# Optimization experiments

Measured on AMD Instinct MI355X. Metric: run time of the kernel, lower is better.

The kernel has to match this reference:

```python
import jax, jax.numpy as jnp
import numpy as np

R, C = 30, 56
N = R * C  # 1680
K = 0.005
PRCN = 15
ALPHA = 1.0
BETA = 1.0


def setup_inputs() -> dict:
    key = jax.random.key(0)
    k1, k2 = jax.random.split(key)
    net_in = jax.random.normal(k1, (2 * N,), dtype=jnp.float32)
    # Recurrent connectivity matrix (learned weight in the original, loaded from .mat)
    J = jax.random.normal(k2, (N, N), dtype=jnp.float32) / np.float32(np.sqrt(N))
    return {"net_in": net_in, "J": J}


def reference(net_in, J):
    Iext = net_in[:N].reshape(R, C)
    r0 = net_in[N:2 * N].reshape(R, C)

    def step(r, _):
        # 4-way chunked mm + cat in the original == single matvec J @ r_flat
        temp = (J @ r.reshape(N)).reshape(R, C)
        U = ALPHA * (BETA * temp) + ALPHA * Iext
        sq = jnp.square(0.2 * U)
        recSum = jnp.sum(K * sq)
        # (0.2*U)^2 * (0.04 / recSum) / 0.04  ==  sq / recSum, kept explicit for fidelity
        r_new = sq * (0.04 / recSum) / 0.04
        return r_new, (U, recSum)

    r_last, (Us, sums) = jax.lax.scan(step, r0, None, length=PRCN - 1)
    return Us[-1], sums[-1], r_last
```

## Files before the change

kernel.cpp:

```cpp
#include <hip/hip_runtime.h>


typedef float f32x4 __attribute__((ext_vector_type(4)));

#define N      1680
#define NV4    420
#define NSTEP  14
#define GBLK   105
#define RPB    16
#define RPW    4

__device__ __forceinline__ void load7_llc(
    const f32x4* p0, const f32x4* p1, const f32x4* p2, const f32x4* p3,
    const f32x4* p4, const f32x4* p5, const f32x4* p6,
    f32x4& v0, f32x4& v1, f32x4& v2, f32x4& v3,
    f32x4& v4, f32x4& v5, f32x4& v6)
{
    asm volatile(
        "global_load_dwordx4 %0, %7, off sc0 sc1\n\t"
        "global_load_dwordx4 %1, %8, off sc0 sc1\n\t"
        "global_load_dwordx4 %2, %9, off sc0 sc1\n\t"
        "global_load_dwordx4 %3, %10, off sc0 sc1\n\t"
        "global_load_dwordx4 %4, %11, off sc0 sc1\n\t"
        "global_load_dwordx4 %5, %12, off sc0 sc1\n\t"
        "global_load_dwordx4 %6, %13, off sc0 sc1\n\t"
        "s_waitcnt vmcnt(0)"
        : "=&v"(v0), "=&v"(v1), "=&v"(v2), "=&v"(v3),
          "=&v"(v4), "=&v"(v5), "=&v"(v6)
        : "v"(p0), "v"(p1), "v"(p2), "v"(p3), "v"(p4), "v"(p5), "v"(p6)
        : "memory");
}

__device__ __forceinline__ void llc_store4(f32x4* p, f32x4 v) {
    asm volatile("global_store_dwordx4 %0, %1, off sc0 sc1"
                 :: "v"(p), "v"(v) : "memory");
}

__device__ __forceinline__ f32x4 vmin4(f32x4 a, f32x4 b) {
    f32x4 r;
    r[0] = fminf(a[0], b[0]); r[1] = fminf(a[1], b[1]);
    r[2] = fminf(a[2], b[2]); r[3] = fminf(a[3], b[3]);
    return r;
}

__global__ __launch_bounds__(256, 1) void fused_recur(
    const float* __restrict__ J,
    const float* __restrict__ net_in,
    float* __restrict__ out,
    float* __restrict__ ws)
{
    f32x4* bufs = (f32x4*)ws;

    const int tid  = threadIdx.x;
    const int lane = tid & 63;
    const int wave = tid >> 6;
    const int row0 = (int)blockIdx.x * RPB + wave * RPW;

    f32x4 Jr[RPW][7];
    #pragma unroll
    for (int m = 0; m < RPW; ++m) {
        const f32x4* Jrow = (const f32x4*)(J + (size_t)(row0 + m) * N);
        #pragma unroll
        for (int k = 0; k < 7; ++k) {
            const int idx = lane + 64 * k;
            Jr[m][k] = (idx < NV4) ? Jrow[idx] : (f32x4)0.f;
        }
    }

    float iext[RPW];
    #pragma unroll
    for (int m = 0; m < RPW; ++m) iext[m] = net_in[row0 + m];

    float Uv[RPW], Qv[RPW];

    #pragma unroll 1
    for (int t = 0; t < NSTEP; ++t) {
        #pragma unroll
        for (int m = 0; m < RPW; ++m)
            #pragma unroll
            for (int k = 0; k < 7; ++k)
                asm volatile("" : "+v"(Jr[m][k]));

        f32x4 rv[7];
        float psum = 0.0f;

        if (t == 0) {
            const f32x4* r0 = (const f32x4*)(net_in + N);
            #pragma unroll
            for (int k = 0; k < 7; ++k) {
                const int idx = lane + 64 * k;
                rv[k] = (idx < NV4) ? r0[idx] : (f32x4)0.f;
            }
        } else {
            const f32x4* base = bufs + (size_t)(t - 1) * NV4;
            const f32x4* q0 = base + (lane);
            const f32x4* q1 = base + (lane + 64);
            const f32x4* q2 = base + (lane + 128);
            const f32x4* q3 = base + (lane + 192);
            const f32x4* q4 = base + (lane + 256);
            const f32x4* q5 = base + (lane + 320);
            const f32x4* q6 = (lane < 36) ? (base + lane + 384) : base;
            for (;;) {
                load7_llc(q0, q1, q2, q3, q4, q5, q6,
                          rv[0], rv[1], rv[2], rv[3], rv[4], rv[5], rv[6]);
                f32x4 m0 = vmin4(vmin4(rv[0], rv[1]), vmin4(rv[2], rv[3]));
                f32x4 m1 = vmin4(vmin4(rv[4], rv[5]), rv[6]);
                f32x4 mm = vmin4(m0, m1);
                const float mn = fminf(fminf(mm[0], mm[1]), fminf(mm[2], mm[3]));
                if (mn >= 0.0f) break;
            }
            if (lane >= 36) rv[6] = (f32x4)0.f;
            #pragma unroll
            for (int k = 0; k < 7; ++k)
                psum += (rv[k][0] + rv[k][1]) + (rv[k][2] + rv[k][3]);
        }

        float red[5];
        #pragma unroll
        for (int m = 0; m < RPW; ++m) {
            float acc = 0.f;
            #pragma unroll
            for (int k = 0; k < 7; ++k) {
                acc += Jr[m][k][0] * rv[k][0];
                acc += Jr[m][k][1] * rv[k][1];
                acc += Jr[m][k][2] * rv[k][2];
                acc += Jr[m][k][3] * rv[k][3];
            }
            red[m] = acc;
        }
        red[4] = psum;
        #pragma unroll
        for (int off = 32; off; off >>= 1) {
            #pragma unroll
            for (int i = 0; i < 5; ++i) red[i] += __shfl_xor(red[i], off, 64);
        }
        const float s = (t == 0) ? 1.0f : 0.005f * red[4];

        #pragma unroll
        for (int m = 0; m < RPW; ++m) {
            const float U  = red[m] / s + iext[m];
            const float u2 = 0.2f * U;
            Uv[m] = U;
            Qv[m] = u2 * u2;
        }

        if (lane == 0) {
            f32x4 pub = { Qv[0], Qv[1], Qv[2], Qv[3] };
            llc_store4(bufs + (size_t)t * NV4 + (row0 >> 2), pub);
        }
    }

    float s13;
    {
        const f32x4* base = bufs + (size_t)(NSTEP - 1) * NV4;
        const f32x4* q0 = base + (lane);
        const f32x4* q1 = base + (lane + 64);
        const f32x4* q2 = base + (lane + 128);
        const f32x4* q3 = base + (lane + 192);
        const f32x4* q4 = base + (lane + 256);
        const f32x4* q5 = base + (lane + 320);
        const f32x4* q6 = (lane < 36) ? (base + lane + 384) : base;
        f32x4 rv[7];
        for (;;) {
            load7_llc(q0, q1, q2, q3, q4, q5, q6,
                      rv[0], rv[1], rv[2], rv[3], rv[4], rv[5], rv[6]);
            f32x4 m0 = vmin4(vmin4(rv[0], rv[1]), vmin4(rv[2], rv[3]));
            f32x4 m1 = vmin4(vmin4(rv[4], rv[5]), rv[6]);
            f32x4 mm = vmin4(m0, m1);
            const float mn = fminf(fminf(mm[0], mm[1]), fminf(mm[2], mm[3]));
            if (mn >= 0.0f) break;
        }
        if (lane >= 36) rv[6] = (f32x4)0.f;
        float psum = 0.f;
        #pragma unroll
        for (int k = 0; k < 7; ++k)
            psum += (rv[k][0] + rv[k][1]) + (rv[k][2] + rv[k][3]);
        #pragma unroll
        for (int off = 32; off; off >>= 1) psum += __shfl_xor(psum, off, 64);
        s13 = 0.005f * psum;
    }

    if (lane == 0) {
        f32x4 u4 = { Uv[0], Uv[1], Uv[2], Uv[3] };
        *(f32x4*)(out + row0) = u4;
    }
    if (lane < RPW) {
        const float q = (lane == 0) ? Qv[0] : (lane == 1) ? Qv[1]
                       : (lane == 2) ? Qv[2] : Qv[3];
        out[N + 1 + row0 + lane] = q / s13;
    }
    if (blockIdx.x == 0 && tid == 0) out[N] = s13;
}

extern "C" void kernel_launch(void* const* d_in, const int* in_sizes, int n_in,
                              void* d_out, int out_size, void* d_ws, size_t ws_size,
                              hipStream_t stream) {
    const float* net_in = (const float*)d_in[0];
    const float* J      = (const float*)d_in[1];
    hipMemsetAsync(d_ws, 0xBF, (size_t)NSTEP * NV4 * sizeof(f32x4), stream);
    fused_recur<<<GBLK, 256, 0, stream>>>(J, net_in, (float*)d_out, (float*)d_ws);
}
```

Baseline: 117.1 us.

## Consume published state chunks incrementally while spinning instead of waiting for all

The spin-wait on the previous step's published state now tracks readiness per 16-byte chunk with a pending bitmask. Each chunk's dot-product and sum contributions are folded in as soon as it is valid, so the matvec overlaps with waiting for slower blocks, and an s_sleep is added between polls. Other changes: J rows are loaded with inline asm, the register-pinning asm barrier is dropped, and the division is replaced by a reciprocal multiply. The risks are more register pressure from the accumulators and rounding that differs slightly from the old order.

```diff
diff --git a/kernel.cpp b/kernel.cpp
--- a/kernel.cpp
+++ b/kernel.cpp
@@ -9,6 +9,26 @@
 #define GBLK   105
 #define RPB    16
 #define RPW    4
+
+__device__ __forceinline__ void jload7(
+    const f32x4* p0, const f32x4* p1, const f32x4* p2, const f32x4* p3,
+    const f32x4* p4, const f32x4* p5, const f32x4* p6,
+    f32x4& v0, f32x4& v1, f32x4& v2, f32x4& v3,
+    f32x4& v4, f32x4& v5, f32x4& v6)
+{
+    asm volatile(
+        "global_load_dwordx4 %0, %7, off\n\t"
+        "global_load_dwordx4 %1, %8, off\n\t"
+        "global_load_dwordx4 %2, %9, off\n\t"
+        "global_load_dwordx4 %3, %10, off\n\t"
+        "global_load_dwordx4 %4, %11, off\n\t"
+        "global_load_dwordx4 %5, %12, off\n\t"
+        "global_load_dwordx4 %6, %13, off\n\t"
+        "s_waitcnt vmcnt(0)"
+        : "=&v"(v0), "=&v"(v1), "=&v"(v2), "=&v"(v3),
+          "=&v"(v4), "=&v"(v5), "=&v"(v6)
+        : "v"(p0), "v"(p1), "v"(p2), "v"(p3), "v"(p4), "v"(p5), "v"(p6));
+}
 
 __device__ __forceinline__ void load7_llc(
     const f32x4* p0, const f32x4* p1, const f32x4* p2, const f32x4* p3,
@@ -36,13 +56,6 @@
                  :: "v"(p), "v"(v) : "memory");
 }
 
-__device__ __forceinline__ f32x4 vmin4(f32x4 a, f32x4 b) {
-    f32x4 r;
-    r[0] = fminf(a[0], b[0]); r[1] = fminf(a[1], b[1]);
-    r[2] = fminf(a[2], b[2]); r[3] = fminf(a[3], b[3]);
-    return r;
-}
-
 __global__ __launch_bounds__(256, 1) void fused_recur(
     const float* __restrict__ J,
     const float* __restrict__ net_in,
@@ -56,15 +69,17 @@
     const int wave = tid >> 6;
     const int row0 = (int)blockIdx.x * RPB + wave * RPW;
 
+    const unsigned pend0 = (lane < 36) ? 0x7Fu : 0x3Fu;
+
     f32x4 Jr[RPW][7];
     #pragma unroll
     for (int m = 0; m < RPW; ++m) {
-        const f32x4* Jrow = (const f32x4*)(J + (size_t)(row0 + m) * N);
-        #pragma unroll
-        for (int k = 0; k < 7; ++k) {
-            const int idx = lane + 64 * k;
-            Jr[m][k] = (idx < NV4) ? Jrow[idx] : (f32x4)0.f;
-        }
+        const f32x4* jb = (const f32x4*)(J + (size_t)(row0 + m) * N);
+        jload7(jb + lane,       jb + lane + 64,  jb + lane + 128,
+               jb + lane + 192, jb + lane + 256, jb + lane + 320,
+               (lane < 36) ? (jb + lane + 384) : jb,
+               Jr[m][0], Jr[m][1], Jr[m][2], Jr[m][3],
+               Jr[m][4], Jr[m][5], Jr[m][6]);
     }
 
     float iext[RPW];
@@ -75,13 +90,9 @@
 
     #pragma unroll 1
     for (int t = 0; t < NSTEP; ++t) {
-        #pragma unroll
-        for (int m = 0; m < RPW; ++m)
-            #pragma unroll
-            for (int k = 0; k < 7; ++k)
-                asm volatile("" : "+v"(Jr[m][k]));
-
-        f32x4 rv[7];
+        f32x4 acc[RPW];
+        #pragma unroll
+        for (int m = 0; m < RPW; ++m) acc[m] = (f32x4)0.f;
         float psum = 0.0f;
 
         if (t == 0) {
@@ -89,56 +100,69 @@
             #pragma unroll
             for (int k = 0; k < 7; ++k) {
                 const int idx = lane + 64 * k;
-                rv[k] = (idx < NV4) ? r0[idx] : (f32x4)0.f;
+                const f32x4 q = (idx < NV4) ? r0[idx] : (f32x4)0.f;
+                #pragma unroll
+                for (int m = 0; m < RPW; ++m) {
+                    acc[m][0] += Jr[m][k][0] * q[0];
+                    acc[m][1] += Jr[m][k][1] * q[1];
+                    acc[m][2] += Jr[m][k][2] * q[2];
+                    acc[m][3] += Jr[m][k][3] * q[3];
+                }
             }
         } else {
             const f32x4* base = bufs + (size_t)(t - 1) * NV4;
-            const f32x4* q0 = base + (lane);
-            const f32x4* q1 = base + (lane + 64);
-            const f32x4* q2 = base + (lane + 128);
-            const f32x4* q3 = base + (lane + 192);
-            const f32x4* q4 = base + (lane + 256);
-            const f32x4* q5 = base + (lane + 320);
+            const f32x4* q0 = base + lane;
+            const f32x4* q1 = base + lane + 64;
+            const f32x4* q2 = base + lane + 128;
+            const f32x4* q3 = base + lane + 192;
+            const f32x4* q4 = base + lane + 256;
+            const f32x4* q5 = base + lane + 320;
             const f32x4* q6 = (lane < 36) ? (base + lane + 384) : base;
+
+            unsigned pend = pend0;
             for (;;) {
+                f32x4 rv[7];
                 load7_llc(q0, q1, q2, q3, q4, q5, q6,
                           rv[0], rv[1], rv[2], rv[3], rv[4], rv[5], rv[6]);
-                f32x4 m0 = vmin4(vmin4(rv[0], rv[1]), vmin4(rv[2], rv[3]));
-                f32x4 m1 = vmin4(vmin4(rv[4], rv[5]), rv[6]);
-                f32x4 mm = vmin4(m0, m1);
-                const float mn = fminf(fminf(mm[0], mm[1]), fminf(mm[2], mm[3]));
-                if (mn >= 0.0f) break;
+                #pragma unroll
+                for (int k = 0; k < 7; ++k) {
+                    if ((pend >> k) & 1u) {
+                        const f32x4 q = rv[k];
+                        const float mn = fminf(fminf(q[0], q[1]),
+                                               fminf(q[2], q[3]));
+                        if (mn >= 0.0f) {
+                            #pragma unroll
+                            for (int m = 0; m < RPW; ++m) {
+                                acc[m][0] += Jr[m][k][0] * q[0];
+                                acc[m][1] += Jr[m][k][1] * q[1];
+                                acc[m][2] += Jr[m][k][2] * q[2];
+                                acc[m][3] += Jr[m][k][3] * q[3];
+                            }
+                            psum += (q[0] + q[1]) + (q[2] + q[3]);
+                            pend &= ~(1u << k);
+                        }
+                    }
+                }
+                if (!__any((int)pend)) break;
+                __builtin_amdgcn_s_sleep(1);
             }
-            if (lane >= 36) rv[6] = (f32x4)0.f;
-            #pragma unroll
-            for (int k = 0; k < 7; ++k)
-                psum += (rv[k][0] + rv[k][1]) + (rv[k][2] + rv[k][3]);
         }
 
         float red[5];
         #pragma unroll
-        for (int m = 0; m < RPW; ++m) {
-            float acc = 0.f;
-            #pragma unroll
-            for (int k = 0; k < 7; ++k) {
-                acc += Jr[m][k][0] * rv[k][0];
-                acc += Jr[m][k][1] * rv[k][1];
-                acc += Jr[m][k][2] * rv[k][2];
-                acc += Jr[m][k][3] * rv[k][3];
-            }
-            red[m] = acc;
-        }
+        for (int m = 0; m < RPW; ++m)
+            red[m] = (acc[m][0] + acc[m][1]) + (acc[m][2] + acc[m][3]);
         red[4] = psum;
         #pragma unroll
         for (int off = 32; off; off >>= 1) {
             #pragma unroll
             for (int i = 0; i < 5; ++i) red[i] += __shfl_xor(red[i], off, 64);
         }
-        const float s = (t == 0) ? 1.0f : 0.005f * red[4];
+        const float inv = (t == 0) ? 1.0f : 1.0f / (0.005f * red[4]);
 
         #pragma unroll
         for (int m = 0; m < RPW; ++m) {
-            const float U  = red[m] / s + iext[m];
+            const float U  = red[m] * inv + iext[m];
             const float u2 = 0.2f * U;
             Uv[m] = U;
             Qv[m] = u2 * u2;
@@ -153,28 +177,35 @@
     float s13;
     {
         const f32x4* base = bufs + (size_t)(NSTEP - 1) * NV4;
-        const f32x4* q0 = base + (lane);
-        const f32x4* q1 = base + (lane + 64);
-        const f32x4* q2 = base + (lane + 128);
-        const f32x4* q3 = base + (lane + 192);
-        const f32x4* q4 = base + (lane + 256);
-        const f32x4* q5 = base + (lane + 320);
+        const f32x4* q0 = base + lane;
+        const f32x4* q1 = base + lane + 64;
+        const f32x4* q2 = base + lane + 128;
+        const f32x4* q3 = base + lane + 192;
+        const f32x4* q4 = base + lane + 256;
+        const f32x4* q5 = base + lane + 320;
         const f32x4* q6 = (lane < 36) ? (base + lane + 384) : base;
-        f32x4 rv[7];
+
+        unsigned pend = pend0;
+        float psum = 0.0f;
         for (;;) {
+            f32x4 rv[7];
             load7_llc(q0, q1, q2, q3, q4, q5, q6,
                       rv[0], rv[1], rv[2], rv[3], rv[4], rv[5], rv[6]);
-            f32x4 m0 = vmin4(vmin4(rv[0], rv[1]), vmin4(rv[2], rv[3]));
-            f32x4 m1 = vmin4(vmin4(rv[4], rv[5]), rv[6]);
-            f32x4 mm = vmin4(m0, m1);
-            const float mn = fminf(fminf(mm[0], mm[1]), fminf(mm[2], mm[3]));
-            if (mn >= 0.0f) break;
-        }
-        if (lane >= 36) rv[6] = (f32x4)0.f;
-        float psum = 0.f;
-        #pragma unroll
-        for (int k = 0; k < 7; ++k)
-            psum += (rv[k][0] + rv[k][1]) + (rv[k][2] + rv[k][3]);
+            #pragma unroll
+            for (int k = 0; k < 7; ++k) {
+                if ((pend >> k) & 1u) {
+                    const f32x4 q = rv[k];
+                    const float mn = fminf(fminf(q[0], q[1]),
+                                           fminf(q[2], q[3]));
+                    if (mn >= 0.0f) {
+                        psum += (q[0] + q[1]) + (q[2] + q[3]);
+                        pend &= ~(1u << k);
+                    }
+                }
+            }
+            if (!__any((int)pend)) break;
+            __builtin_amdgcn_s_sleep(1);
+        }
         #pragma unroll
         for (int off = 32; off; off >>= 1) psum += __shfl_xor(psum, off, 64);
         s13 = 0.005f * psum;
```

Result: slower. 122.4 us (+4.5%).
